# Kernel optimization log

Hardware: AMD Instinct MI355X
Metric: run time of the kernel (lower is better)

## Reference

```python
import jax, jax.numpy as jnp
import numpy as np

GRID_SIZE = 5
SPLINE_ORDER = 3
EPS = 1e-5


def make_grid(in_features):
    # efficient-kan: grid_range=[-1,1], points from -order..grid_size+order
    h = 2.0 / GRID_SIZE
    g = jnp.arange(-SPLINE_ORDER, GRID_SIZE + SPLINE_ORDER + 1, dtype=jnp.float32) * h - 1.0
    return jnp.tile(g[None, :], (in_features, 1))  # [in, grid_size + 2*order + 1]


def b_splines(x, grid):
    # x: [B, in], grid: [in, G] -> bases: [B, in, grid_size + order]
    xg = x[:, :, None]
    bases = ((xg >= grid[:, :-1]) & (xg < grid[:, 1:])).astype(x.dtype)
    for k in range(1, SPLINE_ORDER + 1):
        left = (xg - grid[:, : -(k + 1)]) / (grid[:, k:-1] - grid[:, : -(k + 1)])
        right = (grid[:, k + 1:] - xg) / (grid[:, k + 1:] - grid[:, 1:-k])
        bases = left * bases[:, :, :-1] + right * bases[:, :, 1:]
    return bases


def kan_linear(x, grid, base_w, spline_w, spline_scaler):
    # base path: silu(x) @ base_w.T ; spline path: bsplines(x) contracted with scaled spline weight
    base_out = jnp.einsum('bi,oi->bo', jax.nn.silu(x), base_w)
    bases = b_splines(x, grid)  # [B, in, C]
    sw = spline_w * spline_scaler[:, :, None]  # [out, in, C]
    spline_out = jnp.einsum('bic,oic->bo', bases, sw)
    return base_out + spline_out


def layer_norm(x, w, b):
    mu = jnp.mean(x, axis=-1, keepdims=True)
    var = jnp.mean(jnp.square(x - mu), axis=-1, keepdims=True)
    return (x - mu) * jax.lax.rsqrt(var + EPS) * w + b


def setup_inputs() -> dict:
    key = jax.random.key(0)
    ks = jax.random.split(key, 8)
    B, F, H, E = 65536, 32, 64, 64
    OUT = E * F  # 2048
    C = GRID_SIZE + SPLINE_ORDER  # 8 coeffs per edge
    x = jax.random.normal(ks[0], (B, F), dtype=jnp.float32)
    return {
        'x': x,
        'ln_w': jnp.ones((F,), jnp.float32),
        'ln_b': jnp.zeros((F,), jnp.float32),
        'bw1': jax.random.normal(ks[1], (H, F), jnp.float32) * 0.1,
        'sw1': jax.random.normal(ks[2], (H, F, C), jnp.float32) * 0.1,
        'ss1': jax.random.normal(ks[3], (H, F), jnp.float32) * 0.1 + 1.0,
        'bw2': jax.random.normal(ks[4], (OUT, H), jnp.float32) * 0.1,
        'sw2': jax.random.normal(ks[5], (OUT, H, C), jnp.float32) * 0.1,
        'ss2': jax.random.normal(ks[6], (OUT, H), jnp.float32) * 0.1 + 1.0,
        'grid1': make_grid(F),
        'grid2': make_grid(H),
    }


def reference(x, ln_w, ln_b, bw1, sw1, ss1, bw2, sw2, ss2, grid1, grid2):
    h = layer_norm(x, ln_w, ln_b)
    h = kan_linear(h, grid1, bw1, sw1, ss1)   # [B, 64]
    out = kan_linear(h, grid2, bw2, sw2, ss2)  # [B, 2048]
    return out
```

## Files before the change

### kernel.cpp

```cpp
#include <hip/hip_runtime.h>
#include <stdint.h>

#define BATCH   65536
#define FIN     32
#define HID     64
#define NOUT    2048
#define NC      8
#define NF      9
#define K1      288
#define K2      576

#define BM      256
#define BN      256
#define BK      32
#define KT      18
#define NBUF    4

typedef __bf16 bf16x8 __attribute__((ext_vector_type(8)));
typedef float f32x4 __attribute__((ext_vector_type(4)));

__device__ __forceinline__ uint16_t f2bf(float f) {
    uint32_t u = __builtin_bit_cast(uint32_t, f);
    uint32_t r = (u + 0x7fffu + ((u >> 16) & 1u)) >> 16;
    return (uint16_t)r;
}
__device__ __forceinline__ float silu_f(float v) {
    return v / (1.f + __expf(-v));
}

__device__ __forceinline__ void bspline8u(float xv, float out[8]) {
    float s = (xv + 2.2f) * 2.5f;
    int c = (int)floorf(s);
    float gc = (float)(c - 3) * 0.4f - 1.0f;
    float u = (xv - gc) * 2.5f;
    float u1 = 1.f - u;
    float uu = u * u, u3 = uu * u;
    float w0 = u1 * u1 * u1 * (1.f / 6.f);
    float w1 = (3.f * u3 - 6.f * uu + 4.f) * (1.f / 6.f);
    float w2 = (-3.f * u3 + 3.f * uu + 3.f * u + 1.f) * (1.f / 6.f);
    float w3 = u3 * (1.f / 6.f);
#pragma unroll
    for (int t = 0; t < 8; t++) {
        int d = c - t;
        out[t] = (d == 0) ? w3 : (d == 1) ? w2 : (d == 2) ? w1 : (d == 3) ? w0 : 0.f;
    }
}

__global__ void pack_w1(const float* __restrict__ bw1, const float* __restrict__ sw1,
                        const float* __restrict__ ss1, uint16_t* __restrict__ w1L) {
    int idx = blockIdx.x * 256 + threadIdx.x;
    if (idx >= 64 * K1) return;
    int o = idx / K1, k = idx % K1;
    int i = k / 9, j = k % 9;
    float v = (j == 0) ? bw1[o * FIN + i]
                       : sw1[(o * FIN + i) * NC + (j - 1)] * ss1[o * FIN + i];
    w1L[idx] = f2bf(v);
}

__global__ void pack_w2(const float* __restrict__ bw2, const float* __restrict__ sw2,
                        const float* __restrict__ ss2, uint16_t* __restrict__ w2p) {
    int idx = blockIdx.x * 256 + threadIdx.x;
    if (idx >= NOUT * K2) return;
    int n = idx / K2, k = idx % K2;
    int j = k >> 6, i = k & 63;
    float v = (j == 0) ? bw2[n * HID + i]
                       : sw2[(n * HID + i) * NC + (j - 1)] * ss2[n * HID + i];
    w2p[idx] = f2bf(v);
}

#define FBR   64
#define A1LD  296
__global__ __launch_bounds__(256) void featurize(
    const float* __restrict__ x, const float* __restrict__ lnw, const float* __restrict__ lnb,
    const uint16_t* __restrict__ w1L, uint16_t* __restrict__ a2) {

    __shared__ __align__(16) uint16_t w1s[64 * A1LD];
    __shared__ __align__(16) uint16_t a1s[FBR * A1LD];

    const int tid = threadIdx.x;
    const int wv = tid >> 6, lane = tid & 63;
    const int rowBase = blockIdx.x * FBR;

#pragma unroll
    for (int t = 0; t < 9; ++t) {
        int idx = t * 256 + tid;
        int o = idx / 36, cc = idx % 36;
        uint4 v = *(const uint4*)(w1L + idx * 8);
        *(uint4*)&w1s[o * A1LD + cc * 8] = v;
    }

    const int prow = tid >> 2, pq = tid & 3;
    const float* xp = x + (size_t)(rowBase + prow) * FIN + pq * 8;
    float xv[8];
    *(float4*)&xv[0] = ((const float4*)xp)[0];
    *(float4*)&xv[4] = ((const float4*)xp)[1];
    float s = 0.f, s2 = 0.f;
#pragma unroll
    for (int j = 0; j < 8; j++) { s += xv[j]; s2 += xv[j] * xv[j]; }
    s += __shfl_xor(s, 1);  s2 += __shfl_xor(s2, 1);
    s += __shfl_xor(s, 2);  s2 += __shfl_xor(s2, 2);
    const float mu = s * (1.f / 32.f);
    const float var = s2 * (1.f / 32.f) - mu * mu;
    const float rstd = rsqrtf(var + 1e-5f);

    float wl[8], bl[8];
    *(float4*)&wl[0] = ((const float4*)(lnw + pq * 8))[0];
    *(float4*)&wl[4] = ((const float4*)(lnw + pq * 8))[1];
    *(float4*)&bl[0] = ((const float4*)(lnb + pq * 8))[0];
    *(float4*)&bl[4] = ((const float4*)(lnb + pq * 8))[1];

    __align__(16) uint16_t tmp[72];
#pragma unroll
    for (int ii = 0; ii < 8; ii++) {
        float xn = (xv[ii] - mu) * rstd * wl[ii] + bl[ii];
        tmp[ii * 9] = f2bf(silu_f(xn));
        float bs[8];
        bspline8u(xn, bs);
#pragma unroll
        for (int j = 0; j < 8; j++) tmp[ii * 9 + 1 + j] = f2bf(bs[j]);
    }
    {
        uint16_t* dst = &a1s[prow * A1LD + pq * 72];
#pragma unroll
        for (int q = 0; q < 9; q++) *(uint4*)(dst + q * 8) = *(const uint4*)&tmp[q * 8];
    }
    __syncthreads();

    f32x4 acc[4];
#pragma unroll
    for (int n = 0; n < 4; n++) acc[n] = (f32x4){0.f, 0.f, 0.f, 0.f};
    const int arow = wv * 16 + (lane & 15);
    const int koff = (lane >> 4) * 8;
#pragma unroll
    for (int ks = 0; ks < 9; ++ks) {
        bf16x8 af = *(const bf16x8*)&a1s[arow * A1LD + ks * 32 + koff];
#pragma unroll
        for (int n = 0; n < 4; n++) {
            bf16x8 bv = *(const bf16x8*)&w1s[(n * 16 + (lane & 15)) * A1LD + ks * 32 + koff];
            acc[n] = __builtin_amdgcn_mfma_f32_16x16x32_bf16(af, bv, acc[n], 0, 0, 0);
        }
    }

    const int r0 = wv * 16 + ((lane >> 4) << 2);
    const int cb = lane & 15;
#pragma unroll
    for (int n = 0; n < 4; n++)
#pragma unroll
        for (int r = 0; r < 4; r++) {
            float h = acc[n][r];
            float o9[9];
            o9[0] = silu_f(h);
            bspline8u(h, &o9[1]);
            uint16_t* op = a2 + (size_t)(rowBase + r0 + r) * K2 + n * 16 + cb;
#pragma unroll
            for (int j = 0; j < 9; j++)
                __builtin_nontemporal_store(f2bf(o9[j]), op + j * 64);
        }
}

__device__ __forceinline__ void gload16(const uint16_t* g, const uint16_t* l) {
    __builtin_amdgcn_global_load_lds(
        (const __attribute__((address_space(1))) void*)g,
        (__attribute__((address_space(3))) void*)l, 16, 0, 0);
}

__global__ __launch_bounds__(512, 2) void gemm2_kernel(const uint16_t* __restrict__ A,
                                                       const uint16_t* __restrict__ Bt,
                                                       float* __restrict__ C) {
    __shared__ __align__(16) uint16_t lds[NBUF][2][BM * BK];

    const int tid = threadIdx.x;
    const int wv = tid >> 6, lane = tid & 63;
    const int wr = wv >> 2, wc = wv & 3;

    const uint32_t bid = blockIdx.x;
    const uint32_t wk = (bid & 7u) * 256u + (bid >> 3);
    const uint32_t ntile = wk & 7u, mtile = wk >> 3;

    const int srow = tid >> 2;
    const int scol = (((tid & 3) ^ ((tid >> 3) & 3)) << 3);
    const uint16_t* gA = A  + (size_t)(mtile * BM + srow) * K2 + scol;
    const uint16_t* gB = Bt + (size_t)(ntile * BN + srow) * K2 + scol;

#define STAGE_A(b, kt) do { \
    gload16(gA + (kt) * BK,                    &lds[b][0][wv * 512]); \
    gload16(gA + (size_t)128 * K2 + (kt) * BK, &lds[b][0][4096 + wv * 512]); } while (0)
#define STAGE_B(b, kt) do { \
    gload16(gB + (kt) * BK,                    &lds[b][1][wv * 512]); \
    gload16(gB + (size_t)128 * K2 + (kt) * BK, &lds[b][1][4096 + wv * 512]); } while (0)

    const int slot8 = (((lane >> 4) ^ ((lane >> 1) & 3)) << 3);
    const int aoff = (wr * 128 + (lane & 15)) * BK + slot8;
    const int boff = (wc * 64  + (lane & 15)) * BK + slot8;

    f32x4 acc[8][4];
#pragma unroll
    for (int m = 0; m < 8; m++)
#pragma unroll
        for (int n = 0; n < 4; n++) acc[m][n] = (f32x4){0.f, 0.f, 0.f, 0.f};

    STAGE_A(0, 0); STAGE_B(0, 0);
    STAGE_A(1, 1); STAGE_B(1, 1);
    STAGE_A(2, 2); STAGE_B(2, 2);
    asm volatile("s_waitcnt vmcnt(8)" ::: "memory");
    asm volatile("s_barrier" ::: "memory");

    for (int t = 0; t < KT; ++t) {
        const int b = t & 3;
        const uint16_t* As = &lds[b][0][0];
        const uint16_t* Bs = &lds[b][1][0];
        bf16x8 bv[4], af[4], ag[4];

#pragma unroll
        for (int n = 0; n < 4; ++n) bv[n] = *(const bf16x8*)&Bs[boff + n * 512];
#pragma unroll
        for (int m = 0; m < 4; ++m) af[m] = *(const bf16x8*)&As[aoff + m * 512];
        if (t < KT - 3) STAGE_A((t + 3) & 3, t + 3);
        __builtin_amdgcn_s_setprio(1);
#pragma unroll
        for (int m = 0; m < 4; ++m)
#pragma unroll
            for (int n = 0; n < 4; ++n)
                acc[m][n] = __builtin_amdgcn_mfma_f32_16x16x32_bf16(af[m], bv[n], acc[m][n], 0, 0, 0);
        __builtin_amdgcn_s_setprio(0);

#pragma unroll
        for (int m = 0; m < 4; ++m) ag[m] = *(const bf16x8*)&As[aoff + (m + 4) * 512];
        if (t < KT - 3) STAGE_B((t + 3) & 3, t + 3);
        __builtin_amdgcn_s_setprio(1);
#pragma unroll
        for (int m = 0; m < 4; ++m)
#pragma unroll
            for (int n = 0; n < 4; ++n)
                acc[m + 4][n] = __builtin_amdgcn_mfma_f32_16x16x32_bf16(ag[m], bv[n], acc[m + 4][n], 0, 0, 0);
        __builtin_amdgcn_s_setprio(0);

        if (t < KT - 3)       asm volatile("s_waitcnt vmcnt(8)" ::: "memory");
        else if (t == KT - 3) asm volatile("s_waitcnt vmcnt(4)" ::: "memory");
        else if (t <  KT - 1) asm volatile("s_waitcnt vmcnt(0)" ::: "memory");
        asm volatile("s_barrier" ::: "memory");
    }
#undef STAGE_A
#undef STAGE_B

    const int crow0 = (int)mtile * BM + wr * 128 + ((lane >> 4) << 2);
    const int ccol0 = (int)ntile * BN + wc * 64 + (lane & 15);
#pragma unroll
    for (int m = 0; m < 8; ++m)
#pragma unroll
        for (int n = 0; n < 4; ++n) {
            float* cp = C + (size_t)(crow0 + m * 16) * NOUT + ccol0 + n * 16;
#pragma unroll
            for (int r = 0; r < 4; ++r)
                __builtin_nontemporal_store(acc[m][n][r], cp + (size_t)r * NOUT);
        }
}

extern "C" void kernel_launch(void* const* d_in, const int* in_sizes, int n_in,
                              void* d_out, int out_size, void* d_ws, size_t ws_size,
                              hipStream_t stream) {
    const float* x    = (const float*)d_in[0];
    const float* lnw  = (const float*)d_in[1];
    const float* lnb  = (const float*)d_in[2];
    const float* bw1  = (const float*)d_in[3];
    const float* sw1  = (const float*)d_in[4];
    const float* ss1  = (const float*)d_in[5];
    const float* bw2  = (const float*)d_in[6];
    const float* sw2  = (const float*)d_in[7];
    const float* ss2  = (const float*)d_in[8];

    char* ws = (char*)d_ws;
    uint16_t* w1L = (uint16_t*)ws;
    uint16_t* w2p = (uint16_t*)(ws + 65536);
    uint16_t* a2  = (uint16_t*)(ws + 65536 + 2359296);
    float* out = (float*)d_out;

    pack_w1<<<dim3(72), dim3(256), 0, stream>>>(bw1, sw1, ss1, w1L);
    pack_w2<<<dim3((NOUT * K2 + 255) / 256), dim3(256), 0, stream>>>(bw2, sw2, ss2, w2p);
    featurize<<<dim3(BATCH / FBR), dim3(256), 0, stream>>>(x, lnw, lnb, w1L, a2);
    gemm2_kernel<<<dim3((BATCH / BM) * (NOUT / BN)), dim3(512), 0, stream>>>(a2, w2p, out);
}
```

Baseline: 348.2 us.

## Restructure GEMM2 main loop with B-fragment prefetch and split barriers

Reworks the gemm2 K-loop so all A fragments for a tile are read from LDS up front, B fragments for the next tile are prefetched into registers during the current tile, and the wait/barrier points are split around the two MFMA halves. The loop is also fully unrolled. Separately, nontemporal stores are replaced by ordinary stores for both the intermediate A2 buffer and the final output. The aim is to hide LDS read latency behind MFMA work and let A2 writes stay in cache for the following GEMM. In exchange it adds three barriers per iteration, raises register pressure from the extra fragment registers, and changes the waitcnt accounting, which risks stalls or a hazard on the buffer being refilled.

Result: faster. 282.4 us (-18.9%).

```diff
diff --git a/kernel.cpp b/kernel.cpp
--- a/kernel.cpp
+++ b/kernel.cpp
@@ -153,8 +153,7 @@
             bspline8u(h, &o9[1]);
             uint16_t* op = a2 + (size_t)(rowBase + r0 + r) * K2 + n * 16 + cb;
 #pragma unroll
-            for (int j = 0; j < 9; j++)
-                __builtin_nontemporal_store(f2bf(o9[j]), op + j * 64);
+            for (int j = 0; j < 9; j++) op[j * 64] = f2bf(o9[j]);
         }
 }
 
@@ -205,40 +204,55 @@
     asm volatile("s_waitcnt vmcnt(8)" ::: "memory");
     asm volatile("s_barrier" ::: "memory");
 
+    bf16x8 bvc[4];
+#pragma unroll
+    for (int n = 0; n < 4; ++n) bvc[n] = *(const bf16x8*)&lds[0][1][boff + n * 512];
+
+#pragma unroll
     for (int t = 0; t < KT; ++t) {
         const int b = t & 3;
-        const uint16_t* As = &lds[b][0][0];
-        const uint16_t* Bs = &lds[b][1][0];
-        bf16x8 bv[4], af[4], ag[4];
-
-#pragma unroll
-        for (int n = 0; n < 4; ++n) bv[n] = *(const bf16x8*)&Bs[boff + n * 512];
-#pragma unroll
-        for (int m = 0; m < 4; ++m) af[m] = *(const bf16x8*)&As[aoff + m * 512];
-        if (t < KT - 3) STAGE_A((t + 3) & 3, t + 3);
+        bf16x8 afc[4], afB[4], bvn[4];
+
+#pragma unroll
+        for (int m = 0; m < 4; ++m) afc[m] = *(const bf16x8*)&lds[b][0][aoff + m * 512];
+#pragma unroll
+        for (int m = 0; m < 4; ++m) afB[m] = *(const bf16x8*)&lds[b][0][aoff + (m + 4) * 512];
+        if (t + 3 < KT) STAGE_A((t + 3) & 3, t + 3);
+        if (t <= KT - 4)      asm volatile("s_waitcnt vmcnt(6)" ::: "memory");
+        else if (t == KT - 3) asm volatile("s_waitcnt vmcnt(4)" ::: "memory");
+        else if (t == KT - 2) asm volatile("s_waitcnt vmcnt(0)" ::: "memory");
+        asm volatile("s_barrier" ::: "memory");
+
         __builtin_amdgcn_s_setprio(1);
 #pragma unroll
         for (int m = 0; m < 4; ++m)
 #pragma unroll
             for (int n = 0; n < 4; ++n)
-                acc[m][n] = __builtin_amdgcn_mfma_f32_16x16x32_bf16(af[m], bv[n], acc[m][n], 0, 0, 0);
+                acc[m][n] = __builtin_amdgcn_mfma_f32_16x16x32_bf16(afc[m], bvc[n], acc[m][n], 0, 0, 0);
         __builtin_amdgcn_s_setprio(0);
-
-#pragma unroll
-        for (int m = 0; m < 4; ++m) ag[m] = *(const bf16x8*)&As[aoff + (m + 4) * 512];
-        if (t < KT - 3) STAGE_B((t + 3) & 3, t + 3);
+        asm volatile("s_barrier" ::: "memory");
+
+        if (t < KT - 1) {
+#pragma unroll
+            for (int n = 0; n < 4; ++n)
+                bvn[n] = *(const bf16x8*)&lds[(t + 1) & 3][1][boff + n * 512];
+        }
+        if (t + 3 < KT) STAGE_B((t + 3) & 3, t + 3);
+        asm volatile("s_barrier" ::: "memory");
+
         __builtin_amdgcn_s_setprio(1);
 #pragma unroll
         for (int m = 0; m < 4; ++m)
 #pragma unroll
             for (int n = 0; n < 4; ++n)
-                acc[m + 4][n] = __builtin_amdgcn_mfma_f32_16x16x32_bf16(ag[m], bv[n], acc[m + 4][n], 0, 0, 0);
+                acc[m + 4][n] = __builtin_amdgcn_mfma_f32_16x16x32_bf16(afB[m], bvc[n], acc[m + 4][n], 0, 0, 0);
         __builtin_amdgcn_s_setprio(0);
 
-        if (t < KT - 3)       asm volatile("s_waitcnt vmcnt(8)" ::: "memory");
-        else if (t == KT - 3) asm volatile("s_waitcnt vmcnt(4)" ::: "memory");
-        else if (t <  KT - 1) asm volatile("s_waitcnt vmcnt(0)" ::: "memory");
-        asm volatile("s_barrier" ::: "memory");
+        if (t < KT - 1) {
+            asm volatile("s_barrier" ::: "memory");
+#pragma unroll
+            for (int n = 0; n < 4; ++n) bvc[n] = bvn[n];
+        }
     }
 #undef STAGE_A
 #undef STAGE_B
@@ -251,8 +265,7 @@
         for (int n = 0; n < 4; ++n) {
             float* cp = C + (size_t)(crow0 + m * 16) * NOUT + ccol0 + n * 16;
 #pragma unroll
-            for (int r = 0; r < 4; ++r)
-                __builtin_nontemporal_store(acc[m][n][r], cp + (size_t)r * NOUT);
+            for (int r = 0; r < 4; ++r) cp[(size_t)r * NOUT] = acc[m][n][r];
         }
 }
 
```
